# Kernel tuning notes

Hardware: AMD Instinct MI355X
Metric: run time of the kernel (lower is better)

## Reference

```python
import jax, jax.numpy as jnp
import numpy as np

K = 40  # kNN neighbors (num_points arg)
B, N = 4, 4096

def _bn(x, g, b, axes):
    # training-mode BatchNorm over all axes except channel axis 1
    m = jnp.mean(x, axes, keepdims=True)
    v = jnp.var(x, axes, keepdims=True)
    sh = [1] * x.ndim
    sh[1] = -1
    return (x - m) / jnp.sqrt(v + 1e-5) * g.reshape(sh) + b.reshape(sh)

def _knn(x, k):
    # x: [B, C, N] -> idx [B, N, k]; same math as torch: topk of -||xi-xj||^2
    xx = jnp.sum(x * x, axis=1)                       # [B, N]
    inner = jnp.einsum('bcn,bcm->bnm', x, x)          # [B, N, N]
    neg_d2 = 2.0 * inner - xx[:, :, None] - xx[:, None, :]
    return jax.lax.top_k(neg_d2, k)[1]

def _graph_feature(x, k):
    # EdgeConv feature: concat(neighbor - center, center) -> [B, 2C, N, k]
    idx = jax.lax.stop_gradient(_knn(x, k))           # torch computes idx under no_grad
    xt = jnp.transpose(x, (0, 2, 1))                  # [B, N, C]
    nbr = jax.vmap(lambda f, i: f[i])(xt, idx)        # [B, N, k, C] gather
    ctr = xt[:, :, None, :]
    feat = jnp.concatenate([nbr - ctr, jnp.broadcast_to(ctr, nbr.shape)], axis=-1)
    return jnp.transpose(feat, (0, 3, 1, 2))

def _edge_block(x, W, b, g, e):
    f = _graph_feature(x, K)
    h = jnp.einsum('bcnk,oc->bonk', f, W) + b[None, :, None, None]  # 1x1 Conv2d
    h = jax.nn.leaky_relu(_bn(h, g, e, (0, 2, 3)), 0.2)
    return jnp.max(h, axis=-1)                        # max over k neighbors -> [B, Cout, N]

def _forward(x, w1, b1, g1, e1, w2, b2, g2, e2, w3, b3, g3, e3, w4, b4, g4, e4,
             w5, b5, g5, e5, tw, tb, tg, te, f1w, f1b, f1g, f1e,
             f2w, f2b, f2g, f2e, f3w, f3b):
    x1 = _edge_block(x,  w1, b1, g1, e1)              # [B,64,N]
    x2 = _edge_block(x1, w2, b2, g2, e2)              # [B,64,N]
    x3 = _edge_block(x2, w3, b3, g3, e3)              # [B,128,N]
    x4 = _edge_block(x3, w4, b4, g4, e4)              # [B,256,N]
    cat = jnp.concatenate([x1, x2, x3, x4], axis=1)   # [B,512,N]
    feat = jax.nn.leaky_relu(
        _bn(jnp.einsum('bcn,oc->bon', cat, w5) + b5[None, :, None], g5, e5, (0, 2)), 0.2)
    # TRANS head: Conv1d(1024,1024) -> global max -> MLP 1024-512-256-12 -> 4x4
    h = jax.nn.relu(_bn(jnp.einsum('bcn,oc->bon', feat, tw) + tb[None, :, None], tg, te, (0, 2)))
    h = jnp.max(h, axis=2)                            # [B,1024]
    h = jax.nn.relu(_bn(h @ f1w.T + f1b, f1g, f1e, (0,)))
    h = jax.nn.relu(_bn(h @ f2w.T + f2b, f2g, f2e, (0,)))
    h = h @ f3w.T + f3b                               # [B,12]
    iden = jnp.array([1, 0, 0, 0, 0, 1, 0, 0, 0, 0, 1, 0], jnp.float32)
    h = h + iden[None, :]
    app = jnp.broadcast_to(jnp.array([0, 0, 0, 1], jnp.float32)[None, :], (h.shape[0], 4))
    return jnp.concatenate([h, app], axis=1).reshape(-1, 4, 4)


def setup_inputs() -> dict:
    key = jax.random.key(0)
    ks = jax.random.split(key, 16)
    f32 = jnp.float32
    def W(i, shape, s=0.05):
        return jax.random.normal(ks[i], shape, f32) * s
    def bn_p(c):
        return jnp.ones(c, f32), jnp.zeros(c, f32)
    g1, e1 = bn_p(64); g2, e2 = bn_p(64); g3, e3 = bn_p(128); g4, e4 = bn_p(256)
    g5, e5 = bn_p(1024); tg, te = bn_p(1024); f1g, f1e = bn_p(512); f2g, f2e = bn_p(256)
    return {
        'x': jax.random.normal(ks[0], (B, 3, N), f32),
        'w1': W(1, (64, 6)),    'b1': jnp.zeros(64, f32),  'g1': g1, 'e1': e1,
        'w2': W(2, (64, 128)),  'b2': jnp.zeros(64, f32),  'g2': g2, 'e2': e2,
        'w3': W(3, (128, 128)), 'b3': jnp.zeros(128, f32), 'g3': g3, 'e3': e3,
        'w4': W(4, (256, 256)), 'b4': jnp.zeros(256, f32), 'g4': g4, 'e4': e4,
        'w5': W(5, (1024, 512)), 'b5': jnp.zeros(1024, f32), 'g5': g5, 'e5': e5,
        'tw': W(6, (1024, 1024)), 'tb': jnp.zeros(1024, f32), 'tg': tg, 'te': te,
        'f1w': W(7, (512, 1024)), 'f1b': jnp.zeros(512, f32), 'f1g': f1g, 'f1e': f1e,
        'f2w': W(8, (256, 512)),  'f2b': jnp.zeros(256, f32), 'f2g': f2g, 'f2e': f2e,
        'f3w': W(9, (12, 256)),   'f3b': jnp.zeros(12, f32),
    }


def reference(x, w1, b1, g1, e1, w2, b2, g2, e2, w3, b3, g3, e3, w4, b4, g4, e4,
              w5, b5, g5, e5, tw, tb, tg, te, f1w, f1b, f1g, f1e,
              f2w, f2b, f2g, f2e, f3w, f3b):
    return _forward(x, w1, b1, g1, e1, w2, b2, g2, e2, w3, b3, g3, e3, w4, b4, g4, e4,
                    w5, b5, g5, e5, tw, tb, tg, te, f1w, f1b, f1g, f1e,
                    f2w, f2b, f2g, f2e, f3w, f3b)
```

## Files before the change

### kernel.cpp

```cpp
#include <hip/hip_runtime.h>

#define BB 4
#define NN 4096
#define KK 40

#define NEG_FLT (-3.402823466e38f)
#define POS_FLT (3.402823466e38f)

typedef __attribute__((ext_vector_type(8))) short short8;
typedef __attribute__((ext_vector_type(4))) float f32x4;

__device__ __forceinline__ float lrelu02(float v){ return v > 0.f ? v : 0.2f*v; }
__device__ __forceinline__ int f2ord(float f){ int u = __float_as_int(f); return u >= 0 ? u : (u ^ 0x7fffffff); }
__device__ __forceinline__ unsigned ordu(float f){
  unsigned u = __float_as_uint(f);
  return (u & 0x80000000u) ? ~u : (u | 0x80000000u);
}
__device__ __forceinline__ unsigned long long packkey(float v, int m){
  return ((unsigned long long)ordu(v) << 32) | (unsigned)(~m);
}
__device__ __forceinline__ unsigned short f2bf(float f){
  unsigned u = __float_as_uint(f);
  unsigned r = u + 0x7fffu + ((u>>16)&1u);
  return (unsigned short)(r>>16);
}

template<int C>
__global__ void xx_kernel(const float* __restrict__ x, float* __restrict__ xx){
  int i = blockIdx.x*blockDim.x + threadIdx.x;
  if(i >= BB*NN) return;
  int b = i / NN, n = i % NN;
  const float* xb = x + (size_t)b*C*NN + n;
  float s = 0.f;
  #pragma unroll
  for(int c=0;c<C;c++){ float v = xb[(size_t)c*NN]; s += v*v; }
  xx[i] = s;
}

template<int C>
__global__ __launch_bounds__(256)
void dist_kernel(const float* __restrict__ xb, const float* __restrict__ xx,
                 float* __restrict__ dist){
  __shared__ float As[32][68];
  __shared__ float Bs[32][68];
  const int n0 = blockIdx.y*64, m0 = blockIdx.x*64;
  const int tid = threadIdx.x;
  const int tx = tid & 15, ty = tid >> 4;
  const int lr = tid >> 3, lc0 = (tid & 7)*8;
  float acc[4][4] = {};
  for(int kt=0; kt<C; kt+=32){
    const float* an = xb + (size_t)(kt+lr)*NN + n0 + lc0;
    const float* am = xb + (size_t)(kt+lr)*NN + m0 + lc0;
    *(float4*)&As[lr][lc0]   = *(const float4*)an;
    *(float4*)&As[lr][lc0+4] = *(const float4*)(an+4);
    *(float4*)&Bs[lr][lc0]   = *(const float4*)am;
    *(float4*)&Bs[lr][lc0+4] = *(const float4*)(am+4);
    __syncthreads();
    #pragma unroll
    for(int cc=0;cc<32;cc++){
      float4 av = *(const float4*)&As[cc][ty*4];
      float4 bv = *(const float4*)&Bs[cc][tx*4];
      float a0=av.x,a1=av.y,a2=av.z,a3=av.w;
      float b0=bv.x,b1=bv.y,b2=bv.z,b3=bv.w;
      acc[0][0]+=a0*b0; acc[0][1]+=a0*b1; acc[0][2]+=a0*b2; acc[0][3]+=a0*b3;
      acc[1][0]+=a1*b0; acc[1][1]+=a1*b1; acc[1][2]+=a1*b2; acc[1][3]+=a1*b3;
      acc[2][0]+=a2*b0; acc[2][1]+=a2*b1; acc[2][2]+=a2*b2; acc[2][3]+=a2*b3;
      acc[3][0]+=a3*b0; acc[3][1]+=a3*b1; acc[3][2]+=a3*b2; acc[3][3]+=a3*b3;
    }
    __syncthreads();
  }
  float4 xmv = *(const float4*)(xx + m0 + tx*4);
  float xm0=xmv.x, xm1=xmv.y, xm2=xmv.z, xm3=xmv.w;
  #pragma unroll
  for(int i=0;i<4;i++){
    int n = n0 + ty*4 + i;
    float xn = xx[n];
    float4 r;
    r.x = 2.f*acc[i][0] - xn - xm0;
    r.y = 2.f*acc[i][1] - xn - xm1;
    r.z = 2.f*acc[i][2] - xn - xm2;
    r.w = 2.f*acc[i][3] - xn - xm3;
    *(float4*)(dist + (size_t)n*NN + m0 + tx*4) = r;
  }
}

__global__ __launch_bounds__(256)
void dist3_kernel(const float* __restrict__ xb, const float* __restrict__ xx,
                  float* __restrict__ dist){
  int n = blockIdx.y;
  int m0 = (blockIdx.x*256 + threadIdx.x)*4;
  float c0 = xb[n], c1 = xb[NN+n], c2 = xb[2*NN+n];
  float xn = xx[n];
  float4 a = *(const float4*)(xb + m0);
  float4 b = *(const float4*)(xb + NN + m0);
  float4 c = *(const float4*)(xb + 2*NN + m0);
  float4 xm = *(const float4*)(xx + m0);
  float4 r;
  { float s = c0*a.x; s += c1*b.x; s += c2*c.x; r.x = 2.f*s - xn - xm.x; }
  { float s = c0*a.y; s += c1*b.y; s += c2*c.y; r.y = 2.f*s - xn - xm.y; }
  { float s = c0*a.z; s += c1*b.z; s += c2*c.z; r.z = 2.f*s - xn - xm.z; }
  { float s = c0*a.w; s += c1*b.w; s += c2*c.w; r.w = 2.f*s - xn - xm.w; }
  *(float4*)(dist + (size_t)n*NN + m0) = r;
}

#define INSQ(vf, mi) do{ \
  unsigned long long _pk = packkey((vf),(mi)); \
  if(_pk > t7){ \
    unsigned long long _lo; \
    _lo = _pk < t0 ? _pk : t0;  t0 = _pk > t0 ? _pk : t0;  _pk = _lo; \
    _lo = _pk < t1 ? _pk : t1;  t1 = _pk > t1 ? _pk : t1;  _pk = _lo; \
    _lo = _pk < t2 ? _pk : t2;  t2 = _pk > t2 ? _pk : t2;  _pk = _lo; \
    _lo = _pk < t3 ? _pk : t3;  t3 = _pk > t3 ? _pk : t3;  _pk = _lo; \
    _lo = _pk < t4 ? _pk : t4;  t4 = _pk > t4 ? _pk : t4;  _pk = _lo; \
    _lo = _pk < t5 ? _pk : t5;  t5 = _pk > t5 ? _pk : t5;  _pk = _lo; \
    _lo = _pk < t6 ? _pk : t6;  t6 = _pk > t6 ? _pk : t6;  _pk = _lo; \
    t7 = _pk > t7 ? _pk : t7; \
  } \
}while(0)

__global__ __launch_bounds__(256)
void select_kernel(const float* __restrict__ dA, const float* __restrict__ dB,
                   int* __restrict__ idx){
  const int wid = threadIdx.x >> 6;
  const int lane = threadIdx.x & 63;
  const int r = blockIdx.x*4 + wid;
  const float* row = (r < NN) ? (dA + (size_t)r*NN) : (dB + (size_t)(r-NN)*NN);

  unsigned long long t0=0,t1=0,t2=0,t3=0,t4=0,t5=0,t6=0,t7=0;
  unsigned long long done = 0ull;

  #pragma unroll 4
  for(int j=0;j<16;j++){
    float4 v = *(const float4*)(row + j*256 + lane*4);
    int mb = j*256 + lane*4;
    INSQ(v.x, mb+0); INSQ(v.y, mb+1); INSQ(v.z, mb+2); INSQ(v.w, mb+3);
  }

  __shared__ int outbuf[4][KK];
  #pragma unroll 1
  for(int k=0;k<KK;k++){
    unsigned long long wv = t0;
    #pragma unroll
    for(int off=32; off; off>>=1){
      unsigned long long ov = __shfl_xor(wv, off, 64);
      wv = ov > wv ? ov : wv;
    }
    int m = (int)(~(unsigned)wv);
    if(lane == ((m>>2)&63)){
      done |= 1ull << (((m>>8)<<2) | (m&3));
      t0=t1;t1=t2;t2=t3;t3=t4;t4=t5;t5=t6;t6=t7;t7=0;
      if(t0 == 0ull){
        #pragma unroll 1
        for(int j=0;j<16;j++){
          float4 v = *(const float4*)(row + j*256 + lane*4);
          int mb = j*256 + lane*4;
          if(!((done>>(j*4+0))&1)) INSQ(v.x, mb+0);
          if(!((done>>(j*4+1))&1)) INSQ(v.y, mb+1);
          if(!((done>>(j*4+2))&1)) INSQ(v.z, mb+2);
          if(!((done>>(j*4+3))&1)) INSQ(v.w, mb+3);
        }
      }
    }
    if(lane == 0) outbuf[wid][k] = m;
  }
  if(lane < KK) idx[(size_t)r*KK + lane] = outbuf[wid][lane];
}

template<int C, int O>
__global__ __launch_bounds__(256)
void pq_kernel(const float* __restrict__ x, const float* __restrict__ W,
               const float* __restrict__ bias,
               float* __restrict__ P, float* __restrict__ Q){
  constexpr int G = 256/O;
  constexpr int T = 8/G;
  constexpr int CP = ((C+3)/4)*4;
  __shared__ float xs[8][CP];
  const int tid = threadIdx.x;
  const long long t0b = (long long)blockIdx.x*8;
  const int b = (int)(t0b / NN), n0 = (int)(t0b % NN);
  const float* xb = x + (size_t)b*C*NN;
  for(int e=tid; e<8*C; e+=256){
    int tt = e / C, c = e % C;
    xs[tt][c] = xb[(size_t)c*NN + n0 + tt];
  }
  __syncthreads();

  const int o = tid % O, g = tid / O;
  const float* wrow = W + (size_t)o*2*C;
  float p[T], q[T];
  #pragma unroll
  for(int jt=0;jt<T;jt++){ p[jt]=0.f; q[jt]=0.f; }

  if constexpr(C >= 4){
    for(int c=0;c<C;c+=4){
      float4 w1 = *(const float4*)(wrow + c);
      float4 w2 = *(const float4*)(wrow + C + c);
      float dx = w2.x-w1.x, dy = w2.y-w1.y, dz = w2.z-w1.z, dw = w2.w-w1.w;
      #pragma unroll
      for(int jt=0;jt<T;jt++){
        float4 xv = *(const float4*)&xs[g*T+jt][c];
        p[jt] += w1.x*xv.x; p[jt] += w1.y*xv.y; p[jt] += w1.z*xv.z; p[jt] += w1.w*xv.w;
        q[jt] += dx*xv.x;   q[jt] += dy*xv.y;   q[jt] += dz*xv.z;   q[jt] += dw*xv.w;
      }
    }
  } else {
    float w0=wrow[0], w1v=wrow[1], w2v=wrow[2];
    float d0=wrow[C+0]-w0, d1=wrow[C+1]-w1v, d2=wrow[C+2]-w2v;
    #pragma unroll
    for(int jt=0;jt<T;jt++){
      float a0=xs[g*T+jt][0], a1=xs[g*T+jt][1], a2=xs[g*T+jt][2];
      p[jt] += w0*a0; p[jt] += w1v*a1; p[jt] += w2v*a2;
      q[jt] += d0*a0; q[jt] += d1*a1; q[jt] += d2*a2;
    }
  }
  float bv = bias[o];
  #pragma unroll
  for(int jt=0;jt<T;jt++){
    size_t t = (size_t)t0b + g*T + jt;
    P[t*O + o] = p[jt];
    Q[t*O + o] = q[jt] + bv;
  }
}

template<int O>
__global__ void edge_reduce_kernel(const float* __restrict__ P, const float* __restrict__ Q,
                                   const int* __restrict__ idx,
                                   float* __restrict__ maxh, float* __restrict__ minh,
                                   double* __restrict__ ssum, double* __restrict__ ssq){
  const int o = threadIdx.x;
  const int TN = 8;
  int t0 = blockIdx.x*TN;
  double s = 0.0, s2 = 0.0;
  for(int t=t0;t<t0+TN;t++){
    int bbase = (t/NN)*NN;
    float q = Q[(size_t)t*O + o];
    const int* id = idx + (size_t)t*KK;
    float mx = NEG_FLT, mn = POS_FLT;
    for(int k=0;k<KK;k++){
      int m = id[k];
      float h = P[(size_t)(bbase+m)*O + o] + q;
      mx = fmaxf(mx, h); mn = fminf(mn, h);
      s += (double)h; s2 += (double)h*(double)h;
    }
    maxh[(size_t)t*O + o] = mx;
    minh[(size_t)t*O + o] = mn;
  }
  atomicAdd(&ssum[o], s);
  atomicAdd(&ssq[o], s2);
}

__global__ void finalize_stats(const double* __restrict__ ssum, const double* __restrict__ ssq,
                               const float* __restrict__ g, const float* __restrict__ beta,
                               float* __restrict__ scale, float* __restrict__ shift,
                               int O, double cnt){
  int o = blockIdx.x*blockDim.x + threadIdx.x;
  if(o >= O) return;
  double m = ssum[o]/cnt;
  double v = ssq[o]/cnt - m*m;
  if(v < 0.0) v = 0.0;
  float sc = g[o]/sqrtf((float)v + 1e-5f);
  scale[o] = sc;
  shift[o] = beta[o] - (float)m*sc;
}

template<int O>
__global__ void edge_apply_kernel(const float* __restrict__ maxh, const float* __restrict__ minh,
                                  const float* __restrict__ scale, const float* __restrict__ shift,
                                  float* __restrict__ xout, unsigned short* __restrict__ cat,
                                  int catOff){
  int i = blockIdx.x*blockDim.x + threadIdx.x;
  if(i >= BB*NN*O) return;
  int o = i % O; int t = i / O; int n = t % NN; int b = t / NN;
  float sc = scale[o];
  float v = sc >= 0.f ? maxh[i] : minh[i];
  float y = lrelu02(v*sc + shift[o]);
  xout[((size_t)b*O + o)*NN + n] = y;
  cat[(size_t)t*512 + catOff + o] = f2bf(y);
}

__global__ __launch_bounds__(256)
void gemm_bf16_kernel(const unsigned short* __restrict__ A, const unsigned short* __restrict__ Bw,
                      const float* __restrict__ bias, float* __restrict__ Cout,
                      int M, int Kd, int O){
  __shared__ unsigned short Al[128*72];
  __shared__ unsigned short Bl[128*72];
  const int m0 = blockIdx.x*128, o0 = blockIdx.y*128;
  const int tid = threadIdx.x;
  const int w = tid >> 6, l = tid & 63;
  const int wm = (w>>1)*64, wn = (w&1)*64;
  const int sr = tid >> 1;
  const int sc = (tid & 1)*32;
  const int frow = l & 15, kgrp = (l>>4)*8;
  f32x4 acc[4][4] = {};

  for(int kt=0; kt<Kd; kt+=64){
    const unsigned short* Ap = A  + (size_t)(m0+sr)*Kd + kt + sc;
    const unsigned short* Bp = Bw + (size_t)(o0+sr)*Kd + kt + sc;
    __syncthreads();
    *(short8*)&Al[sr*72 + sc     ] = *(const short8*)(Ap);
    *(short8*)&Al[sr*72 + sc +  8] = *(const short8*)(Ap+8);
    *(short8*)&Al[sr*72 + sc + 16] = *(const short8*)(Ap+16);
    *(short8*)&Al[sr*72 + sc + 24] = *(const short8*)(Ap+24);
    *(short8*)&Bl[sr*72 + sc     ] = *(const short8*)(Bp);
    *(short8*)&Bl[sr*72 + sc +  8] = *(const short8*)(Bp+8);
    *(short8*)&Bl[sr*72 + sc + 16] = *(const short8*)(Bp+16);
    *(short8*)&Bl[sr*72 + sc + 24] = *(const short8*)(Bp+24);
    __syncthreads();
    #pragma unroll
    for(int ks=0; ks<2; ks++){
      short8 af[4], bf[4];
      #pragma unroll
      for(int f=0; f<4; f++){
        af[f] = *(const short8*)&Al[(wm+f*16+frow)*72 + ks*32 + kgrp];
        bf[f] = *(const short8*)&Bl[(wn+f*16+frow)*72 + ks*32 + kgrp];
      }
      #pragma unroll
      for(int i=0;i<4;i++)
        #pragma unroll
        for(int j=0;j<4;j++)
          acc[i][j] = __builtin_amdgcn_mfma_f32_16x16x32_bf16(af[i], bf[j], acc[i][j], 0,0,0);
    }
  }
  const int crow = (l>>4)*4, ccol = l & 15;
  #pragma unroll
  for(int i=0;i<4;i++){
    #pragma unroll
    for(int j=0;j<4;j++){
      int oc = o0 + wn + j*16 + ccol;
      float bv = bias[oc];
      #pragma unroll
      for(int r=0;r<4;r++){
        int mr = m0 + wm + i*16 + crow + r;
        Cout[(size_t)mr*O + oc] = acc[i][j][r] + bv;
      }
    }
  }
}

__global__ void wcvt_kernel(const float* __restrict__ in, unsigned short* __restrict__ out, int n){
  int i = blockIdx.x*blockDim.x + threadIdx.x;
  if(i < n) out[i] = f2bf(in[i]);
}

__global__ void colstats_kernel(const float* __restrict__ H, double* __restrict__ ssum,
                                double* __restrict__ ssq, int O){
  int o  = blockIdx.x*blockDim.x + threadIdx.x;
  int m0 = blockIdx.y*64;
  double s=0.0, s2=0.0;
  for(int m=m0;m<m0+64;m++){
    float h = H[(size_t)m*O + o];
    s += (double)h; s2 += (double)h*(double)h;
  }
  atomicAdd(&ssum[o], s); atomicAdd(&ssq[o], s2);
}

__global__ void bn_lrelu_bf16_kernel(const float* __restrict__ H, const float* __restrict__ scale,
                                     const float* __restrict__ shift, unsigned short* __restrict__ Hb,
                                     int O, long long total){
  long long i = (long long)blockIdx.x*blockDim.x + threadIdx.x;
  if(i >= total) return;
  int o = (int)(i % O);
  Hb[i] = f2bf(lrelu02(H[i]*scale[o] + shift[o]));
}

__global__ void init_minmax_kernel(int* __restrict__ gmax, int* __restrict__ gmin, int n){
  int i = blockIdx.x*blockDim.x + threadIdx.x;
  if(i < n){ gmax[i] = -2147483647-1; gmin[i] = 2147483647; }
}

__global__ void colminmax_kernel(const float* __restrict__ H, int* __restrict__ gmax,
                                 int* __restrict__ gmin, int O){
  int o  = blockIdx.x*blockDim.x + threadIdx.x;
  int b  = blockIdx.y >> 4;
  int nt = blockIdx.y & 15;
  const float* Hp = H + (size_t)(b*NN + nt*256)*O + o;
  float mx = NEG_FLT, mn = POS_FLT;
  for(int i2=0;i2<256;i2++){
    float h = Hp[(size_t)i2*O];
    mx = fmaxf(mx, h); mn = fminf(mn, h);
  }
  atomicMax(&gmax[b*O + o], f2ord(mx));
  atomicMin(&gmin[b*O + o], f2ord(mn));
}

__global__ void t_apply_kernel(const int* __restrict__ gmax, const int* __restrict__ gmin,
                               const float* __restrict__ scale, const float* __restrict__ shift,
                               float* __restrict__ tfeat, int O){
  int i = blockIdx.x*blockDim.x + threadIdx.x;
  if(i >= BB*O) return;
  int o = i % O;
  float sc = scale[o];
  int ov = sc >= 0.f ? gmax[i] : gmin[i];
  float v = __int_as_float(ov >= 0 ? ov : (ov ^ 0x7fffffff));
  float y = v*sc + shift[o];
  tfeat[i] = fmaxf(y, 0.f);
}

__global__ __launch_bounds__(128)
void fc_bn_relu_kernel(const float* __restrict__ X, const float* __restrict__ W,
                       const float* __restrict__ bias, const float* __restrict__ g,
                       const float* __restrict__ beta, float* __restrict__ Y,
                       int Cin, int Cout){
  int j = blockIdx.x;
  __shared__ float red[4][128];
  float a0=0,a1=0,a2=0,a3=0;
  const float* w = W + (size_t)j*Cin;
  for(int c=threadIdx.x;c<Cin;c+=128){
    float wv = w[c];
    a0 += X[c]*wv; a1 += X[Cin+c]*wv; a2 += X[2*Cin+c]*wv; a3 += X[3*Cin+c]*wv;
  }
  red[0][threadIdx.x]=a0; red[1][threadIdx.x]=a1; red[2][threadIdx.x]=a2; red[3][threadIdx.x]=a3;
  __syncthreads();
  for(int s=64;s>=1;s>>=1){
    if(threadIdx.x < s){
      #pragma unroll
      for(int b=0;b<4;b++) red[b][threadIdx.x] += red[b][threadIdx.x+s];
    }
    __syncthreads();
  }
  if(threadIdx.x == 0){
    float h[4];
    #pragma unroll
    for(int b=0;b<4;b++) h[b] = red[b][0] + bias[j];
    float m = 0.25f*(h[0]+h[1]+h[2]+h[3]);
    float var = 0.f;
    #pragma unroll
    for(int b=0;b<4;b++){ float d = h[b]-m; var += d*d; }
    var *= 0.25f;
    float sc = g[j]/sqrtf(var + 1e-5f);
    #pragma unroll
    for(int b=0;b<4;b++){
      float y = (h[b]-m)*sc + beta[j];
      Y[(size_t)b*Cout + j] = fmaxf(y, 0.f);
    }
  }
}

__global__ __launch_bounds__(64)
void fc3_kernel(const float* __restrict__ X, const float* __restrict__ W,
                const float* __restrict__ bias, float* __restrict__ out){
  int t = threadIdx.x; int b = t >> 4; int j = t & 15;
  float v;
  if(j < 12){
    float acc = 0.f;
    const float* w = W + (size_t)j*256;
    const float* xb = X + (size_t)b*256;
    for(int c=0;c<256;c++) acc += xb[c]*w[c];
    v = acc + bias[j];
    if(j==0 || j==5 || j==10) v += 1.f;
  } else {
    v = (j==15) ? 1.f : 0.f;
  }
  out[t] = v;
}

template<int C>
static void run_knn(const float* xin, const float* xxb, float* distA, float* distB,
                    int* idxb, hipStream_t stream){
  for(int half=0; half<2; half++){
    int b0 = half*2;
    for(int j=0;j<2;j++){
      int b = b0 + j;
      float* dd = j==0 ? distA : distB;
      const float* xb = xin + (size_t)b*C*NN;
      const float* xx = xxb + (size_t)b*NN;
      if constexpr(C == 3){
        dist3_kernel<<<dim3(NN/1024, NN), 256, 0, stream>>>(xb, xx, dd);
      } else {
        dist_kernel<C><<<dim3(NN/64, NN/64), 256, 0, stream>>>(xb, xx, dd);
      }
    }
    select_kernel<<<2*NN/4, 256, 0, stream>>>(distA, distB, idxb + (size_t)b0*NN*KK);
  }
}

template<int C, int O>
static void run_edge_block(const float* xin, const float* W, const float* bias,
                           const float* g, const float* e, float* xout, int catOff,
                           float* xxb, int* idxb, float* P, float* Q,
                           float* maxh, float* minh, float* distB,
                           double* ssum, double* ssq,
                           float* scaleb, float* shiftb, unsigned short* catb, hipStream_t stream){
  xx_kernel<C><<<(BB*NN+255)/256, 256, 0, stream>>>(xin, xxb);
  run_knn<C>(xin, xxb, P , distB, idxb, stream);
  pq_kernel<C,O><<<BB*NN/8, 256, 0, stream>>>(xin, W, bias, P, Q);
  hipMemsetAsync(ssum, 0, O*sizeof(double), stream);
  hipMemsetAsync(ssq,  0, O*sizeof(double), stream);
  edge_reduce_kernel<O><<<BB*NN/8, O, 0, stream>>>(P, Q, idxb, maxh, minh, ssum, ssq);
  finalize_stats<<<(O+255)/256, 256, 0, stream>>>(ssum, ssq, g, e, scaleb, shiftb, O, (double)BB*NN*KK);
  edge_apply_kernel<O><<<(BB*NN*O+255)/256, 256, 0, stream>>>(maxh, minh, scaleb, shiftb, xout, catb, catOff);
}

extern "C" void kernel_launch(void* const* d_in, const int* in_sizes, int n_in,
                              void* d_out, int out_size, void* d_ws, size_t ws_size,
                              hipStream_t stream){
  (void)in_sizes; (void)n_in; (void)out_size; (void)ws_size;
  const float* x   = (const float*)d_in[0];
  const float* w1  = (const float*)d_in[1];  const float* b1 = (const float*)d_in[2];
  const float* g1  = (const float*)d_in[3];  const float* e1 = (const float*)d_in[4];
  const float* w2  = (const float*)d_in[5];  const float* b2 = (const float*)d_in[6];
  const float* g2  = (const float*)d_in[7];  const float* e2 = (const float*)d_in[8];
  const float* w3  = (const float*)d_in[9];  const float* b3 = (const float*)d_in[10];
  const float* g3  = (const float*)d_in[11]; const float* e3 = (const float*)d_in[12];
  const float* w4  = (const float*)d_in[13]; const float* b4 = (const float*)d_in[14];
  const float* g4  = (const float*)d_in[15]; const float* e4 = (const float*)d_in[16];
  const float* w5  = (const float*)d_in[17]; const float* b5 = (const float*)d_in[18];
  const float* g5  = (const float*)d_in[19]; const float* e5 = (const float*)d_in[20];
  const float* twp = (const float*)d_in[21]; const float* tbp = (const float*)d_in[22];
  const float* tg  = (const float*)d_in[23]; const float* te  = (const float*)d_in[24];
  const float* f1w = (const float*)d_in[25]; const float* f1b = (const float*)d_in[26];
  const float* f1g = (const float*)d_in[27]; const float* f1e = (const float*)d_in[28];
  const float* f2w = (const float*)d_in[29]; const float* f2b = (const float*)d_in[30];
  const float* f2g = (const float*)d_in[31]; const float* f2e = (const float*)d_in[32];
  const float* f3w = (const float*)d_in[33]; const float* f3b = (const float*)d_in[34];

  char* ws = (char*)d_ws;
  size_t off = 0;
  auto alloc = [&](size_t bytes)->void*{
    void* p = ws + off;
    off += (bytes + 255) & ~(size_t)255;
    return p;
  };
  int*    idxb  = (int*)   alloc((size_t)BB*NN*KK*4);
  float*  xxb   = (float*) alloc((size_t)BB*NN*4);
  float*  x1    = (float*) alloc((size_t)BB*64*NN*4);
  float*  x2    = (float*) alloc((size_t)BB*64*NN*4);
  float*  x3    = (float*) alloc((size_t)BB*128*NN*4);
  float*  x4    = (float*) alloc((size_t)BB*256*NN*4);
  float*  P     = (float*) alloc((size_t)BB*NN*256*4);
  float*  Q     = (float*) alloc((size_t)BB*NN*256*4);
  float*  maxh  = (float*) alloc((size_t)BB*NN*256*4);
  float*  minh  = (float*) alloc((size_t)BB*NN*256*4);
  unsigned short* catb = (unsigned short*) alloc((size_t)BB*NN*512*2);
  float*  h5    = (float*) alloc((size_t)BB*NN*1024*4);
  double* ssum  = (double*)alloc(1024*8);
  double* ssq   = (double*)alloc(1024*8);
  float*  scaleb= (float*) alloc(1024*4);
  float*  shiftb= (float*) alloc(1024*4);
  int*    gmax  = (int*)   alloc((size_t)BB*1024*4);
  int*    gmin  = (int*)   alloc((size_t)BB*1024*4);
  float*  tfeat = (float*) alloc((size_t)BB*1024*4);
  float*  y1    = (float*) alloc((size_t)BB*512*4);
  float*  y2    = (float*) alloc((size_t)BB*256*4);

  unsigned short* w5b  = (unsigned short*)x1;
  unsigned short* twb  = (unsigned short*)x2;
  unsigned short* h5b  = (unsigned short*)maxh;
  float*          h6   = h5;

  run_edge_block<3,  64 >(x,  w1, b1, g1, e1, x1, 0,   xxb, idxb, P, Q, maxh, minh, h5, ssum, ssq, scaleb, shiftb, catb, stream);
  run_edge_block<64, 64 >(x1, w2, b2, g2, e2, x2, 64,  xxb, idxb, P, Q, maxh, minh, h5, ssum, ssq, scaleb, shiftb, catb, stream);
  run_edge_block<64, 128>(x2, w3, b3, g3, e3, x3, 128, xxb, idxb, P, Q, maxh, minh, h5, ssum, ssq, scaleb, shiftb, catb, stream);
  run_edge_block<128,256>(x3, w4, b4, g4, e4, x4, 256, xxb, idxb, P, Q, maxh, minh, h5, ssum, ssq, scaleb, shiftb, catb, stream);

  const int M = BB*NN;
  wcvt_kernel<<<(1024*512 +255)/256, 256, 0, stream>>>(w5,  w5b, 1024*512);
  wcvt_kernel<<<(1024*1024+255)/256, 256, 0, stream>>>(twp, twb, 1024*1024);

  gemm_bf16_kernel<<<dim3(M/128, 1024/128), 256, 0, stream>>>(catb, w5b, b5, h5, M, 512, 1024);
  hipMemsetAsync(ssum, 0, 1024*8, stream);
  hipMemsetAsync(ssq,  0, 1024*8, stream);
  colstats_kernel<<<dim3(1024/256, M/64), 256, 0, stream>>>(h5, ssum, ssq, 1024);
  finalize_stats<<<4, 256, 0, stream>>>(ssum, ssq, g5, e5, scaleb, shiftb, 1024, (double)M);
  bn_lrelu_bf16_kernel<<<(int)(((long long)M*1024+255)/256), 256, 0, stream>>>(h5, scaleb, shiftb, h5b, 1024, (long long)M*1024);

  gemm_bf16_kernel<<<dim3(M/128, 1024/128), 256, 0, stream>>>(h5b, twb, tbp, h6, M, 1024, 1024);
  hipMemsetAsync(ssum, 0, 1024*8, stream);
  hipMemsetAsync(ssq,  0, 1024*8, stream);
  init_minmax_kernel<<<(BB*1024+255)/256, 256, 0, stream>>>(gmax, gmin, BB*1024);
  colstats_kernel<<<dim3(1024/256, M/64), 256, 0, stream>>>(h6, ssum, ssq, 1024);
  colminmax_kernel<<<dim3(1024/256, BB*(NN/256)), 256, 0, stream>>>(h6, gmax, gmin, 1024);
  finalize_stats<<<4, 256, 0, stream>>>(ssum, ssq, tg, te, scaleb, shiftb, 1024, (double)M);
  t_apply_kernel<<<(BB*1024+255)/256, 256, 0, stream>>>(gmax, gmin, scaleb, shiftb, tfeat, 1024);

  fc_bn_relu_kernel<<<512, 128, 0, stream>>>(tfeat, f1w, f1b, f1g, f1e, y1, 1024, 512);
  fc_bn_relu_kernel<<<256, 128, 0, stream>>>(y1, f2w, f2b, f2g, f2e, y2, 512, 256);
  fc3_kernel<<<1, 64, 0, stream>>>(y2, f3w, f3b, (float*)d_out);
}
```

Before: 2.016 ms.

## Enlarge distance GEMM tiles and replace per-point PQ projection with tiled GEMM

The pairwise distance kernel now uses 128x128 output tiles with an 8x8 register tile per thread and a k-step of 16. This raises arithmetic intensity and cuts shared-memory traffic per FMA. The edge-conv projection for C>=32 layers becomes a shared-memory tiled GEMM, fed by a small kernel that pre-transposes the weights into W1 and W2-W1 matrices. Together these replace the old per-thread dot-product loop, at the cost of higher register pressure (64 accumulators) and an extra weight-transform launch per block.

Result: faster. 1.898 ms (-5.9%).

```diff
diff --git a/kernel.cpp b/kernel.cpp
--- a/kernel.cpp
+++ b/kernel.cpp
@@ -41,46 +41,56 @@
 __global__ __launch_bounds__(256)
 void dist_kernel(const float* __restrict__ xb, const float* __restrict__ xx,
                  float* __restrict__ dist){
-  __shared__ float As[32][68];
-  __shared__ float Bs[32][68];
-  const int n0 = blockIdx.y*64, m0 = blockIdx.x*64;
+  __shared__ float As[16][132];
+  __shared__ float Bs[16][132];
+  const int n0 = blockIdx.y*128, m0 = blockIdx.x*128;
   const int tid = threadIdx.x;
   const int tx = tid & 15, ty = tid >> 4;
-  const int lr = tid >> 3, lc0 = (tid & 7)*8;
-  float acc[4][4] = {};
-  for(int kt=0; kt<C; kt+=32){
-    const float* an = xb + (size_t)(kt+lr)*NN + n0 + lc0;
-    const float* am = xb + (size_t)(kt+lr)*NN + m0 + lc0;
-    *(float4*)&As[lr][lc0]   = *(const float4*)an;
-    *(float4*)&As[lr][lc0+4] = *(const float4*)(an+4);
-    *(float4*)&Bs[lr][lc0]   = *(const float4*)am;
-    *(float4*)&Bs[lr][lc0+4] = *(const float4*)(am+4);
+  const int lr = tid >> 4;
+  const int lc0 = (tid & 15)*8;
+  float acc[8][8] = {};
+  for(int kt=0; kt<C; kt+=16){
     __syncthreads();
-    #pragma unroll
-    for(int cc=0;cc<32;cc++){
-      float4 av = *(const float4*)&As[cc][ty*4];
-      float4 bv = *(const float4*)&Bs[cc][tx*4];
-      float a0=av.x,a1=av.y,a2=av.z,a3=av.w;
-      float b0=bv.x,b1=bv.y,b2=bv.z,b3=bv.w;
-      acc[0][0]+=a0*b0; acc[0][1]+=a0*b1; acc[0][2]+=a0*b2; acc[0][3]+=a0*b3;
-      acc[1][0]+=a1*b0; acc[1][1]+=a1*b1; acc[1][2]+=a1*b2; acc[1][3]+=a1*b3;
-      acc[2][0]+=a2*b0; acc[2][1]+=a2*b1; acc[2][2]+=a2*b2; acc[2][3]+=a2*b3;
-      acc[3][0]+=a3*b0; acc[3][1]+=a3*b1; acc[3][2]+=a3*b2; acc[3][3]+=a3*b3;
+    {
+      const float* an = xb + (size_t)(kt+lr)*NN + n0 + lc0;
+      const float* am = xb + (size_t)(kt+lr)*NN + m0 + lc0;
+      *(float4*)&As[lr][lc0]   = *(const float4*)an;
+      *(float4*)&As[lr][lc0+4] = *(const float4*)(an+4);
+      *(float4*)&Bs[lr][lc0]   = *(const float4*)am;
+      *(float4*)&Bs[lr][lc0+4] = *(const float4*)(am+4);
     }
     __syncthreads();
-  }
-  float4 xmv = *(const float4*)(xx + m0 + tx*4);
-  float xm0=xmv.x, xm1=xmv.y, xm2=xmv.z, xm3=xmv.w;
-  #pragma unroll
-  for(int i=0;i<4;i++){
-    int n = n0 + ty*4 + i;
+    #pragma unroll
+    for(int cc=0;cc<16;cc++){
+      float a[8], b[8];
+      *(float4*)&a[0] = *(const float4*)&As[cc][ty*8];
+      *(float4*)&a[4] = *(const float4*)&As[cc][ty*8+4];
+      *(float4*)&b[0] = *(const float4*)&Bs[cc][tx*8];
+      *(float4*)&b[4] = *(const float4*)&Bs[cc][tx*8+4];
+      #pragma unroll
+      for(int i=0;i<8;i++)
+        #pragma unroll
+        for(int j=0;j<8;j++) acc[i][j] += a[i]*b[j];
+    }
+  }
+  float xmv[8];
+  #pragma unroll
+  for(int j=0;j<8;j++) xmv[j] = xx[m0 + tx*8 + j];
+  #pragma unroll
+  for(int i=0;i<8;i++){
+    int n = n0 + ty*8 + i;
     float xn = xx[n];
-    float4 r;
-    r.x = 2.f*acc[i][0] - xn - xm0;
-    r.y = 2.f*acc[i][1] - xn - xm1;
-    r.z = 2.f*acc[i][2] - xn - xm2;
-    r.w = 2.f*acc[i][3] - xn - xm3;
-    *(float4*)(dist + (size_t)n*NN + m0 + tx*4) = r;
+    float4 r0, r1;
+    r0.x = 2.f*acc[i][0] - xn - xmv[0];
+    r0.y = 2.f*acc[i][1] - xn - xmv[1];
+    r0.z = 2.f*acc[i][2] - xn - xmv[2];
+    r0.w = 2.f*acc[i][3] - xn - xmv[3];
+    r1.x = 2.f*acc[i][4] - xn - xmv[4];
+    r1.y = 2.f*acc[i][5] - xn - xmv[5];
+    r1.z = 2.f*acc[i][6] - xn - xmv[6];
+    r1.w = 2.f*acc[i][7] - xn - xmv[7];
+    *(float4*)(dist + (size_t)n*NN + m0 + tx*8)     = r0;
+    *(float4*)(dist + (size_t)n*NN + m0 + tx*8 + 4) = r1;
   }
 }
 
@@ -167,6 +177,74 @@
 }
 
 template<int C, int O>
+__global__ void wt_kernel(const float* __restrict__ w, float* __restrict__ Wt1,
+                          float* __restrict__ Wtd){
+  int i = blockIdx.x*256 + threadIdx.x;
+  if(i >= C*O) return;
+  int c = i / O, o = i % O;
+  float a = w[(size_t)o*2*C + c];
+  float b = w[(size_t)o*2*C + C + c];
+  Wt1[i] = a; Wtd[i] = b - a;
+}
+
+template<int C, int O>
+__global__ __launch_bounds__(256)
+void pq_gemm_kernel(const float* __restrict__ x, const float* __restrict__ Wt1,
+                    const float* __restrict__ Wtd, const float* __restrict__ bias,
+                    float* __restrict__ P, float* __restrict__ Q){
+  __shared__ float Xs[32][68];
+  __shared__ float W1s[32][68];
+  __shared__ float Wds[32][68];
+  const int t0 = blockIdx.x*64;
+  const int o0 = blockIdx.y*64;
+  const int b  = t0 / NN, n0 = t0 % NN;
+  const float* xb = x + (size_t)b*C*NN;
+  const int tid = threadIdx.x;
+  const int tx = tid & 15, ty = tid >> 4;
+  const int lr = tid >> 3, lc0 = (tid & 7)*8;
+  float pa[4][4] = {}, qa[4][4] = {};
+  for(int kt=0; kt<C; kt+=32){
+    __syncthreads();
+    {
+      const float* xs = xb + (size_t)(kt+lr)*NN + n0 + lc0;
+      *(float4*)&Xs[lr][lc0]   = *(const float4*)xs;
+      *(float4*)&Xs[lr][lc0+4] = *(const float4*)(xs+4);
+      const float* w1 = Wt1 + (size_t)(kt+lr)*O + o0 + lc0;
+      *(float4*)&W1s[lr][lc0]   = *(const float4*)w1;
+      *(float4*)&W1s[lr][lc0+4] = *(const float4*)(w1+4);
+      const float* wd = Wtd + (size_t)(kt+lr)*O + o0 + lc0;
+      *(float4*)&Wds[lr][lc0]   = *(const float4*)wd;
+      *(float4*)&Wds[lr][lc0+4] = *(const float4*)(wd+4);
+    }
+    __syncthreads();
+    #pragma unroll
+    for(int cc=0;cc<32;cc++){
+      float a[4], w[4], d[4];
+      *(float4*)a = *(const float4*)&Xs[cc][ty*4];
+      *(float4*)w = *(const float4*)&W1s[cc][tx*4];
+      *(float4*)d = *(const float4*)&Wds[cc][tx*4];
+      #pragma unroll
+      for(int i=0;i<4;i++)
+        #pragma unroll
+        for(int j=0;j<4;j++){
+          pa[i][j] += a[i]*w[j];
+          qa[i][j] += a[i]*d[j];
+        }
+    }
+  }
+  #pragma unroll
+  for(int i=0;i<4;i++){
+    size_t t = (size_t)t0 + ty*4 + i;
+    #pragma unroll
+    for(int j=0;j<4;j++){
+      int o = o0 + tx*4 + j;
+      P[t*O + o] = pa[i][j];
+      Q[t*O + o] = qa[i][j] + bias[o];
+    }
+  }
+}
+
+template<int C, int O>
 __global__ __launch_bounds__(256)
 void pq_kernel(const float* __restrict__ x, const float* __restrict__ W,
                const float* __restrict__ bias,
@@ -191,27 +269,13 @@
   #pragma unroll
   for(int jt=0;jt<T;jt++){ p[jt]=0.f; q[jt]=0.f; }
 
-  if constexpr(C >= 4){
-    for(int c=0;c<C;c+=4){
-      float4 w1 = *(const float4*)(wrow + c);
-      float4 w2 = *(const float4*)(wrow + C + c);
-      float dx = w2.x-w1.x, dy = w2.y-w1.y, dz = w2.z-w1.z, dw = w2.w-w1.w;
-      #pragma unroll
-      for(int jt=0;jt<T;jt++){
-        float4 xv = *(const float4*)&xs[g*T+jt][c];
-        p[jt] += w1.x*xv.x; p[jt] += w1.y*xv.y; p[jt] += w1.z*xv.z; p[jt] += w1.w*xv.w;
-        q[jt] += dx*xv.x;   q[jt] += dy*xv.y;   q[jt] += dz*xv.z;   q[jt] += dw*xv.w;
-      }
-    }
-  } else {
-    float w0=wrow[0], w1v=wrow[1], w2v=wrow[2];
-    float d0=wrow[C+0]-w0, d1=wrow[C+1]-w1v, d2=wrow[C+2]-w2v;
-    #pragma unroll
-    for(int jt=0;jt<T;jt++){
-      float a0=xs[g*T+jt][0], a1=xs[g*T+jt][1], a2=xs[g*T+jt][2];
-      p[jt] += w0*a0; p[jt] += w1v*a1; p[jt] += w2v*a2;
-      q[jt] += d0*a0; q[jt] += d1*a1; q[jt] += d2*a2;
-    }
+  float w0=wrow[0], w1v=wrow[1], w2v=wrow[2];
+  float d0=wrow[C+0]-w0, d1=wrow[C+1]-w1v, d2=wrow[C+2]-w2v;
+  #pragma unroll
+  for(int jt=0;jt<T;jt++){
+    float a0=xs[g*T+jt][0], a1=xs[g*T+jt][1], a2=xs[g*T+jt][2];
+    p[jt] += w0*a0; p[jt] += w1v*a1; p[jt] += w2v*a2;
+    q[jt] += d0*a0; q[jt] += d1*a1; q[jt] += d2*a2;
   }
   float bv = bias[o];
   #pragma unroll
@@ -467,7 +531,7 @@
       if constexpr(C == 3){
         dist3_kernel<<<dim3(NN/1024, NN), 256, 0, stream>>>(xb, xx, dd);
       } else {
-        dist_kernel<C><<<dim3(NN/64, NN/64), 256, 0, stream>>>(xb, xx, dd);
+        dist_kernel<C><<<dim3(NN/128, NN/128), 256, 0, stream>>>(xb, xx, dd);
       }
     }
     select_kernel<<<2*NN/4, 256, 0, stream>>>(distA, distB, idxb + (size_t)b0*NN*KK);
@@ -479,11 +543,17 @@
                            const float* g, const float* e, float* xout, int catOff,
                            float* xxb, int* idxb, float* P, float* Q,
                            float* maxh, float* minh, float* distB,
+                           float* Wt1, float* Wtd,
                            double* ssum, double* ssq,
                            float* scaleb, float* shiftb, unsigned short* catb, hipStream_t stream){
   xx_kernel<C><<<(BB*NN+255)/256, 256, 0, stream>>>(xin, xxb);
   run_knn<C>(xin, xxb, P , distB, idxb, stream);
-  pq_kernel<C,O><<<BB*NN/8, 256, 0, stream>>>(xin, W, bias, P, Q);
+  if constexpr(C >= 32){
+    wt_kernel<C,O><<<(C*O+255)/256, 256, 0, stream>>>(W, Wt1, Wtd);
+    pq_gemm_kernel<C,O><<<dim3(BB*NN/64, O/64), 256, 0, stream>>>(xin, Wt1, Wtd, bias, P, Q);
+  } else {
+    pq_kernel<C,O><<<BB*NN/8, 256, 0, stream>>>(xin, W, bias, P, Q);
+  }
   hipMemsetAsync(ssum, 0, O*sizeof(double), stream);
   hipMemsetAsync(ssq,  0, O*sizeof(double), stream);
   edge_reduce_kernel<O><<<BB*NN/8, O, 0, stream>>>(P, Q, idxb, maxh, minh, ssum, ssq);
@@ -533,6 +603,8 @@
   float*  minh  = (float*) alloc((size_t)BB*NN*256*4);
   unsigned short* catb = (unsigned short*) alloc((size_t)BB*NN*512*2);
   float*  h5    = (float*) alloc((size_t)BB*NN*1024*4);
+  float*  Wt1   = (float*) alloc((size_t)256*128*4);
+  float*  Wtd   = (float*) alloc((size_t)256*128*4);
   double* ssum  = (double*)alloc(1024*8);
   double* ssq   = (double*)alloc(1024*8);
   float*  scaleb= (float*) alloc(1024*4);
@@ -548,10 +620,10 @@
   unsigned short* h5b  = (unsigned short*)maxh;
   float*          h6   = h5;
 
-  run_edge_block<3,  64 >(x,  w1, b1, g1, e1, x1, 0,   xxb, idxb, P, Q, maxh, minh, h5, ssum, ssq, scaleb, shiftb, catb, stream);
-  run_edge_block<64, 64 >(x1, w2, b2, g2, e2, x2, 64,  xxb, idxb, P, Q, maxh, minh, h5, ssum, ssq, scaleb, shiftb, catb, stream);
-  run_edge_block<64, 128>(x2, w3, b3, g3, e3, x3, 128, xxb, idxb, P, Q, maxh, minh, h5, ssum, ssq, scaleb, shiftb, catb, stream);
-  run_edge_block<128,256>(x3, w4, b4, g4, e4, x4, 256, xxb, idxb, P, Q, maxh, minh, h5, ssum, ssq, scaleb, shiftb, catb, stream);
+  run_edge_block<3,  64 >(x,  w1, b1, g1, e1, x1, 0,   xxb, idxb, P, Q, maxh, minh, h5, Wt1, Wtd, ssum, ssq, scaleb, shiftb, catb, stream);
+  run_edge_block<64, 64 >(x1, w2, b2, g2, e2, x2, 64,  xxb, idxb, P, Q, maxh, minh, h5, Wt1, Wtd, ssum, ssq, scaleb, shiftb, catb, stream);
+  run_edge_block<64, 128>(x2, w3, b3, g3, e3, x3, 128, xxb, idxb, P, Q, maxh, minh, h5, Wt1, Wtd, ssum, ssq, scaleb, shiftb, catb, stream);
+  run_edge_block<128,256>(x3, w4, b4, g4, e4, x4, 256, xxb, idxb, P, Q, maxh, minh, h5, Wt1, Wtd, ssum, ssq, scaleb, shiftb, catb, stream);
 
   const int M = BB*NN;
   wcvt_kernel<<<(1024*512 +255)/256, 256, 0, stream>>>(w5,  w5b, 1024*512);
```
